# Optimization experiments

Measured on AMD Instinct MI355X. Metric: run time of the kernel, lower is better.

## Reference

```python
import jax, jax.numpy as jnp
import numpy as np

B, NO, T, SD = 2, 96, 50, 4
NE = NO * (NO - 1)            # 9120 directed edges
F, L = 64, 64                 # filter_dim, latent_dim
K, STRIDE = 8, 3              # num_time_instances, stride (hard-coded in __init__)
NW = (T - K) // STRIDE + 1    # 15 temporal windows


def swish(x):
    return x * jax.nn.sigmoid(x)


def conv1d(x, w, b):
    # x [N, Cin, T], w [Cout, Cin, k], 'same' padding as in nn.Conv1d(padding=k//2)
    k = w.shape[-1]
    y = jax.lax.conv_general_dilated(x, w, (1,), [(k // 2, k // 2)],
                                     dimension_numbers=('NCH', 'OIH', 'NCH'))
    return y + b[None, :, None]


def cond_res_block(x, latent, c1w, c1b, c2w, c2b, l1w, l1b, l2w, l2b):
    # CondResBlock1d (downsample=False): x [B*NE, F, T], latent [B, NE, L]
    l1 = latent @ l1w.T + l1b             # [B, NE, 2F]
    l2 = latent @ l2w.T + l2b
    g1, b1 = l1[..., :F], l1[..., F:]
    g2, b2 = l2[..., :F], l2[..., F:]
    t = x.shape[-1]
    h = conv1d(x, c1w, c1b).reshape(B, NE, F, t)
    h = swish(g1[..., None] * h + b1[..., None]).reshape(B * NE, F, t)
    h = conv1d(h, c2w, c2b).reshape(B, NE, F, t)
    h = swish(g2[..., None] * h + b2[..., None]).reshape(B * NE, F, t)
    return x + h


def cond_mlp_block(x, latent, f1w, f1b, f2w, f2b, l1w, l1b, l2w, l2b):
    # CondMLPResBlock1d, 3-D branch: x [B, NE, F]
    l1 = latent @ l1w.T + l1b
    l2 = latent @ l2w.T + l2b
    h = swish(l1[..., :F] * (x @ f1w.T + f1b) + l1[..., F:])
    h = swish(l2[..., :F] * (h @ f2w.T + f2b) + l2[..., F:])
    return x + h


def setup_inputs() -> dict:
    ks = iter(jax.random.split(jax.random.key(0), 40))

    def rn(shape, scale=1.0):
        return jax.random.normal(next(ks), shape, dtype=jnp.float32) * scale

    return {
        'states': rn((B, NO, T, SD)),
        'latent': rn((B, NE, L), 0.1),
        'cnnbf_w': rn((F, 2 * SD, 3), (2 * SD * 3) ** -0.5),
        'cnnbf_b': jnp.zeros((F,), jnp.float32),
        'rb_conv1_w': rn((2, F, F, 5), (F * 5) ** -0.5),
        'rb_conv1_b': jnp.zeros((2, F), jnp.float32),
        'rb_conv2_w': rn((2, F, F, 5), 1e-5),   # torch init: conv2 std=1e-5
        'rb_conv2_b': jnp.zeros((2, F), jnp.float32),
        'rb_lfc1_w': rn((2, 2 * F, L), L ** -0.5),
        'rb_lfc1_b': jnp.zeros((2, 2 * F), jnp.float32),
        'rb_lfc2_w': rn((2, 2 * F, L), L ** -0.5),
        'rb_lfc2_b': jnp.zeros((2, 2 * F), jnp.float32),
        'mlp1_fc1_w': rn((F, F * K), (F * K) ** -0.5),
        'mlp1_fc1_b': jnp.full((F,), 0.1, jnp.float32),  # MLPBlock bias fill 0.1
        'mlp1_fc2_w': rn((F, F), F ** -0.5),
        'mlp1_fc2_b': jnp.full((F,), 0.1, jnp.float32),
        'ml_fc1_w': rn((3, F, F), 1e-5),        # CondMLPResBlock fc std=1e-5
        'ml_fc1_b': jnp.zeros((3, F), jnp.float32),
        'ml_fc2_w': rn((3, F, F), 1e-5),
        'ml_fc2_b': jnp.zeros((3, F), jnp.float32),
        'ml_lfc1_w': rn((3, 2 * F, L), L ** -0.5),
        'ml_lfc1_b': jnp.zeros((3, 2 * F), jnp.float32),
        'ml_lfc2_w': rn((3, 2 * F, L), L ** -0.5),
        'ml_lfc2_b': jnp.zeros((3, 2 * F), jnp.float32),
        'em_w': rn((1, F), F ** -0.5),
        'em_b': jnp.zeros((1,), jnp.float32),
        'recv_idx': jax.random.randint(next(ks), (NE,), 0, NO, dtype=jnp.int32),
        'send_idx': jax.random.randint(next(ks), (NE,), 0, NO, dtype=jnp.int32),
    }


def reference(states, latent, cnnbf_w, cnnbf_b, rb_conv1_w, rb_conv1_b,
              rb_conv2_w, rb_conv2_b, rb_lfc1_w, rb_lfc1_b, rb_lfc2_w, rb_lfc2_b,
              mlp1_fc1_w, mlp1_fc1_b, mlp1_fc2_w, mlp1_fc2_b,
              ml_fc1_w, ml_fc1_b, ml_fc2_w, ml_fc2_b,
              ml_lfc1_w, ml_lfc1_b, ml_lfc2_w, ml_lfc2_b,
              em_w, em_b, recv_idx, send_idx):
    # node2edge gather: concat receiver/sender node trajectories -> [B, NE, T, 2*SD]
    edges = jnp.concatenate([states[:, recv_idx], states[:, send_idx]], axis=-1)
    x = edges.transpose(0, 1, 3, 2).reshape(B * NE, 2 * SD, T)
    x = swish(conv1d(x, cnnbf_w, cnnbf_b))            # [B*NE, F, T]
    for i in range(2):                                 # layer1/2_cnn_bf
        x = cond_res_block(x, latent, rb_conv1_w[i], rb_conv1_b[i],
                           rb_conv2_w[i], rb_conv2_b[i],
                           rb_lfc1_w[i], rb_lfc1_b[i], rb_lfc2_w[i], rb_lfc2_b[i])
    # temporal unfold into NW windows of K steps with stride STRIDE
    win = jnp.arange(NW)[:, None] * STRIDE + jnp.arange(K)[None, :]  # [NW, K]
    xw = x[:, :, win]                                  # [B*NE, F, NW, K]
    xw = xw.transpose(0, 2, 1, 3).reshape(B, NE, NW, F * K)
    h = swish(xw @ mlp1_fc1_w.T + mlp1_fc1_b)          # MLPBlock (eval: no dropout)
    h = (h @ mlp1_fc2_w.T + mlp1_fc2_b).mean(axis=2)   # pool windows -> [B, NE, F]
    for i in range(3):                                 # layer1/2/3
        h = cond_mlp_block(h, latent, ml_fc1_w[i], ml_fc1_b[i],
                           ml_fc2_w[i], ml_fc2_b[i],
                           ml_lfc1_w[i], ml_lfc1_b[i], ml_lfc2_w[i], ml_lfc2_b[i])
    return (h @ em_w.T + em_b)[..., 0]                 # per-edge energy [B, NE]
```

## Files before the change

kernel.cpp:

```cpp
#include <hip/hip_runtime.h>

#define B_      2
#define NO_     96
#define T_      50
#define SD_     4
#define NE_     (NO_*(NO_-1))
#define F_      64
#define NW_     15

typedef __attribute__((ext_vector_type(8))) short  short8;
typedef __attribute__((ext_vector_type(4))) float  f32x4;
typedef __attribute__((ext_vector_type(2))) float  f32x2;
typedef __attribute__((ext_vector_type(4))) unsigned short u16x4;
typedef __attribute__((ext_vector_type(2))) unsigned int   u32x2;
typedef __attribute__((ext_vector_type(4))) unsigned int   u32x4;

#define E_CONVA 0
#define E_FC1A  81920
#define E_RBL   114688
#define E_CONDP 147456
#define E_FCP   196608
#define E_C0A   225280
#define N_BF16  227328
#define HBAR_F32 115712

#define FI_FC1   10240
#define FI_RBL   14336
#define FI_CONDP 18432
#define FI_FCP   24576
#define FI_C0A   28160

#define XSTRIDE  3456
#define X0OFF    256

#define MFMA(a, b, c) __builtin_amdgcn_mfma_f32_16x16x32_bf16(a, b, c, 0, 0, 0)

__device__ __forceinline__ float swish_(float v) {
    return v * __builtin_amdgcn_rcpf(1.f + __expf(-v));
}
__device__ __forceinline__ f32x2 swish2v(f32x2 v) {
    f32x2 e;
    e.x = __expf(-v.x); e.y = __expf(-v.y);
    f32x2 d = e + (f32x2){1.f, 1.f};
    f32x2 r;
    r.x = __builtin_amdgcn_rcpf(d.x); r.y = __builtin_amdgcn_rcpf(d.y);
    return v * r;
}

__device__ __forceinline__ unsigned short f2bf(float f) {
    unsigned u = __float_as_uint(f);
    u += 0x7FFFu + ((u >> 16) & 1u);
    return (unsigned short)(u >> 16);
}
__device__ __forceinline__ float bf2f(unsigned short u) {
    return __uint_as_float(((unsigned)u) << 16);
}
__device__ __forceinline__ unsigned cvtpk(float lo, float hi) {
    unsigned r;
    asm("v_cvt_pk_bf16_f32 %0, %1, %2" : "=v"(r) : "v"(lo), "v"(hi));
    return r;
}

__global__ void prep_kernel(const float* __restrict__ cnnbf_w,
                            const float* __restrict__ rb1w, const float* __restrict__ rb2w,
                            const float* __restrict__ fc1w, const float* __restrict__ fc2w,
                            const float* __restrict__ rbl1w, const float* __restrict__ rbl2w,
                            const float* __restrict__ mll1w, const float* __restrict__ mll2w,
                            const float* __restrict__ mlf1w, const float* __restrict__ mlf2w,
                            float* __restrict__ ws) {
    int e = blockIdx.x * blockDim.x + threadIdx.x;
    if (e >= N_BF16) return;
    unsigned short* bfp = (unsigned short*)((char*)ws + 8192);
    float v;
    if (e < E_FC1A) {
        int r = e & 511, fid = e >> 9;
        int lane = r >> 3, j = r & 7;
        int kk = fid % 10, m = (fid / 10) & 3, c = fid / 40;
        int fo = m*16 + (lane & 15);
        int kidx = kk*32 + (lane >> 4)*8 + j;
        int k = kidx >> 6, fi = kidx & 63;
        int i = c >> 1;
        const float* src = (c & 1) ? rb2w : rb1w;
        v = src[((i*64 + fo)*64 + fi)*5 + k];
    } else if (e < E_RBL) {
        int e2 = e - E_FC1A;
        int r = e2 & 511, fid = e2 >> 9;
        int lane = r >> 3, j = r & 7;
        int kk = fid & 15, m = fid >> 4;
        int fo = m*16 + (lane & 15);
        int k = kk*32 + (lane >> 4)*8 + j;
        int krow = (k & 63)*8 + (k >> 6);
        v = fc1w[fo*512 + krow];
    } else if (e < E_CONDP) {
        int e3 = e - E_RBL;
        int j = e3 & 7, lane = (e3 >> 3) & 63, fid = e3 >> 9;
        int kk = fid & 1, nt = fid >> 1;
        int rb = nt >> 4, which = (nt >> 3) & 1, ot = nt & 7;
        int o = ot*16 + (lane & 15);
        int k = kk*32 + (lane >> 4)*8 + j;
        const float* src = which ? rbl2w : rbl1w;
        v = src[(rb*128 + o)*64 + k];
    } else if (e < E_FCP) {
        int e4 = e - E_CONDP;
        int r = e4 & 511, fid = e4 >> 9;
        int lane = r >> 3, j = r & 7;
        int kk = fid & 1, nt = (fid >> 1) & 15, mb = fid >> 5;
        int n = nt*16 + (lane & 15);
        int which = n >> 7, o = n & 127;
        int k = kk*32 + (lane >> 4)*8 + j;
        const float* src = which ? mll2w : mll1w;
        v = src[(mb*128 + o)*64 + k];
    } else if (e < E_C0A) {
        int e5 = e - E_FCP;
        int r = e5 & 511, fid = e5 >> 9;
        int lane = r >> 3, j = r & 7;
        int kk = fid & 1, nt = (fid >> 1) & 3, g = fid >> 3;
        int o = nt*16 + (lane & 15);
        int k = kk*32 + (lane >> 4)*8 + j;
        if (g == 0) v = fc2w[o*64 + k];
        else {
            int mb = (g - 1) >> 1;
            const float* src = ((g - 1) & 1) ? mlf2w : mlf1w;
            v = src[(mb*64 + o)*64 + k];
        }
    } else {
        int e6 = e - E_C0A;
        int j = e6 & 7, lane = (e6 >> 3) & 63, m = e6 >> 9;
        int fo = m*16 + (lane & 15);
        int k = (lane >> 4)*8 + j;
        int tap = k >> 3, fi = k & 7;
        v = (tap < 3) ? cnnbf_w[(fo*8 + fi)*3 + tap] : 0.f;
    }
    bfp[e] = f2bf(v);
}

template<bool ISCONV2>
__device__ __forceinline__ void convpass2e(const short8* __restrict__ AF, int fb,
        const unsigned short* __restrict__ Bb, unsigned short* __restrict__ Db,
        const float* __restrict__ cb,
        const float* __restrict__ gv0, const float* __restrict__ bv0,
        const float* __restrict__ gv1, const float* __restrict__ bv1,
        const int (&dixs)[2][2], const int (&ia)[10], const int (&ib)[10],
        bool skip1, int lane, int mi) {
    f32x4 acc[2][4];
#pragma unroll
    for (int ed = 0; ed < 2; ++ed)
#pragma unroll
        for (int q = 0; q < 4; ++q) acc[ed][q] = (f32x4){0.f,0.f,0.f,0.f};
#pragma unroll
    for (int kk = 0; kk < 10; ++kk) {
        short8 a0 = AF[fb + ((mi*2 + 0)*10 + kk)*64 + lane];
        short8 a1 = AF[fb + ((mi*2 + 1)*10 + kk)*64 + lane];
#pragma unroll
        for (int ed = 0; ed < 2; ++ed) {
            const unsigned short* Bs = Bb + ed*XSTRIDE;
            short8 b0 = *(const short8*)&Bs[ia[kk]];
            short8 b1 = *(const short8*)&Bs[ib[kk]];
            acc[ed][0] = MFMA(a0, b0, acc[ed][0]);
            acc[ed][1] = MFMA(a0, b1, acc[ed][1]);
            acc[ed][2] = MFMA(a1, b0, acc[ed][2]);
            acc[ed][3] = MFMA(a1, b1, acc[ed][3]);
        }
    }
#pragma unroll
    for (int ed = 0; ed < 2; ++ed) {
        const float* gv = ed ? gv1 : gv0;
        const float* bv = ed ? bv1 : bv0;
        unsigned short* Dst = Db + ed*XSTRIDE;
#pragma unroll
        for (int a = 0; a < 2; ++a) {
            const int fo0 = (mi*2 + a)*16 + ((lane >> 4))*4;
            const f32x4 cb4 = *(const f32x4*)&cb[fo0];
            const f32x4 g4  = *(const f32x4*)&gv[fo0];
            const f32x4 b4  = *(const f32x4*)&bv[fo0];
            const f32x2 glo = {g4[0], g4[1]}, ghi = {g4[2], g4[3]};
            const f32x2 gcl = __builtin_elementwise_fma(
                (f32x2){cb4[0], cb4[1]}, glo, (f32x2){b4[0], b4[1]});
            const f32x2 gch = __builtin_elementwise_fma(
                (f32x2){cb4[2], cb4[3]}, ghi, (f32x2){b4[2], b4[3]});
#pragma unroll
            for (int n = 0; n < 2; ++n) {
                if (n == 1 && skip1) continue;
                const f32x4 A = acc[ed][a*2 + n];
                f32x2 vlo = __builtin_elementwise_fma((f32x2){A[0], A[1]}, glo, gcl);
                f32x2 vhi = __builtin_elementwise_fma((f32x2){A[2], A[3]}, ghi, gch);
                f32x2 slo = swish2v(vlo);
                f32x2 shi = swish2v(vhi);
                if (ISCONV2) {
                    u16x4 old = *(u16x4*)&Dst[dixs[a][n]];
                    f32x2 olo = {bf2f(old[0]), bf2f(old[1])};
                    f32x2 ohi = {bf2f(old[2]), bf2f(old[3])};
                    slo = slo + olo; shi = shi + ohi;
                }
                *(u32x2*)&Dst[dixs[a][n]] = (u32x2){cvtpk(slo.x, slo.y),
                                                    cvtpk(shi.x, shi.y)};
            }
        }
    }
}

__global__ __launch_bounds__(256, 4) void mega_kernel(
    const float* __restrict__ states, const float* __restrict__ latent,
    const float* __restrict__ cnnbf_b,
    const float* __restrict__ rb_conv1_b, const float* __restrict__ rb_conv2_b,
    const float* __restrict__ rb_lfc1_b, const float* __restrict__ rb_lfc2_b,
    const float* __restrict__ mlp1_fc1_b,
    const int* __restrict__ recv_idx, const int* __restrict__ send_idx,
    const float* __restrict__ ws, float* __restrict__ hbar) {

    const int ge0 = blockIdx.x * 2;
    const int tid  = threadIdx.x;
    const int lane = tid & 63;
    const int wv   = tid >> 6;
    const int row0 = lane & 15, g0 = lane >> 4;
    const int mi = wv & 1, ni = wv >> 1;

    __shared__ __align__(16) unsigned short xTb[2*54*64];
    __shared__ __align__(16) unsigned short hTb[2*54*64];
    __shared__ __align__(16) unsigned short lat_bfb[2*64];
    __shared__ __align__(16) float cond_sb[2*512];

    const unsigned short* bfp = (const unsigned short*)((const char*)ws + 8192);
    const short8* AF = (const short8*)bfp;

    int dixs[2][2];
    const bool skip1 = (ni == 1) && (row0 < 14);
#pragma unroll
    for (int a = 0; a < 2; ++a) {
        const int fo0 = (mi*2 + a)*16 + g0*4;
#pragma unroll
        for (int n = 0; n < 2; ++n) {
            const int t = ((n == 0) ? ni*32 : (ni == 0 ? 16 : 34)) + row0;
            const int rw = t + 2;
            dixs[a][n] = rw*64 + ((((fo0 >> 3) ^ (rw & 7))) << 3) + (fo0 & 7);
        }
    }
    int ia[10], ib[10];
#pragma unroll
    for (int kk = 0; kk < 10; ++kk) {
        const int c  = ((kk & 1) << 2) + g0;
        const int sa = ni*32 + row0 + (kk >> 1);
        ia[kk] = sa*64 + ((c ^ (sa & 7)) << 3);
        if (ni == 0) ib[kk] = ia[kk] + 1024;
        else { const int sb2 = sa + 2; ib[kk] = sb2*64 + ((c ^ (sb2 & 7)) << 3); }
    }

    for (int z = tid; z < 512; z += 256) {
        const int edz = z >> 8, rr = (z >> 6) & 3, cc = z & 63;
        const int row = (rr < 2) ? rr : 50 + rr;
        xTb[edz*XSTRIDE + row*64 + cc] = 0;
        hTb[edz*XSTRIDE + row*64 + cc] = 0;
    }
    if (tid < 8) {
        const int edz = tid >> 2, q = tid & 3;
        const int rz = (q == 0) ? 0 : 50 + q;
        short8 zz = {0,0,0,0,0,0,0,0};
        *(short8*)&hTb[edz*XSTRIDE + X0OFF + rz*8] = zz;
    }
    const int b0_ = ge0 / NE_,       e0_ = ge0 % NE_;
    const int b1_ = (ge0+1) / NE_,   e1_ = (ge0+1) % NE_;
    const int rv0 = recv_idx[e0_], sd0 = send_idx[e0_];
    const int rv1 = recv_idx[e1_], sd1 = send_idx[e1_];
    {
        const int ed = tid >> 7, t = tid & 127;
        if (t < T_) {
            const int bsel = ed ? b1_ : b0_;
            const int rv = ed ? rv1 : rv0, sd = ed ? sd1 : sd0;
            const f32x4 r4 = *(const f32x4*)&states[((bsel*NO_ + rv)*T_ + t)*SD_];
            const f32x4 s4 = *(const f32x4*)&states[((bsel*NO_ + sd)*T_ + t)*SD_];
            u32x4 q4;
            q4[0] = cvtpk(r4[0], r4[1]); q4[1] = cvtpk(r4[2], r4[3]);
            q4[2] = cvtpk(s4[0], s4[1]); q4[3] = cvtpk(s4[2], s4[3]);
            *(u32x4*)&hTb[ed*XSTRIDE + X0OFF + (t + 1)*8] = q4;
        }
    }
    if (tid < 128) {
        const int edz = tid >> 6, c = tid & 63;
        const int bsel = edz ? b1_ : b0_, esel = edz ? e1_ : e0_;
        lat_bfb[edz*64 + c] = f2bf(latent[(bsel*NE_ + esel)*64 + c]);
    }
    __syncthreads();

    {
        const int t0a = ni * 32;
        const int sa = t0a + row0 + g0;
        const int sb = (ni == 0) ? (sa + 16) : (sa + 2);
        short8 a0 = AF[FI_C0A + (mi*2 + 0)*64 + lane];
        short8 a1 = AF[FI_C0A + (mi*2 + 1)*64 + lane];
        const f32x4 z4 = {0.f,0.f,0.f,0.f};
#pragma unroll
        for (int ed = 0; ed < 2; ++ed) {
            const unsigned short* xp = hTb + ed*XSTRIDE + X0OFF;
            short8 b0 = *(const short8*)&xp[sa * 8];
            short8 b1 = *(const short8*)&xp[sb * 8];
            f32x4 c00 = MFMA(a0, b0, z4), c01 = MFMA(a0, b1, z4);
            f32x4 c10 = MFMA(a1, b0, z4), c11 = MFMA(a1, b1, z4);
            unsigned short* xw = xTb + ed*XSTRIDE;
#pragma unroll
            for (int a = 0; a < 2; ++a) {
                const int fo0 = (mi*2 + a)*16 + g0*4;
                const f32x4 cb4 = *(const f32x4*)&cnnbf_b[fo0];
#pragma unroll
                for (int n = 0; n < 2; ++n) {
                    if (n == 1 && skip1) continue;
                    const f32x4 A = (a == 0) ? ((n == 0) ? c00 : c01)
                                             : ((n == 0) ? c10 : c11);
                    f32x2 vlo = (f32x2){A[0], A[1]} + (f32x2){cb4[0], cb4[1]};
                    f32x2 vhi = (f32x2){A[2], A[3]} + (f32x2){cb4[2], cb4[3]};
                    f32x2 slo = swish2v(vlo);
                    f32x2 shi = swish2v(vhi);
                    *(u32x2*)&xw[dixs[a][n]] = (u32x2){cvtpk(slo.x, slo.y),
                                                       cvtpk(shi.x, shi.y)};
                }
            }
        }
        short8 la0_0 = *(const short8*)&lat_bfb[g0 * 8];
        short8 la1_0 = *(const short8*)&lat_bfb[32 + g0 * 8];
        short8 la0_1 = *(const short8*)&lat_bfb[64 + g0 * 8];
        short8 la1_1 = *(const short8*)&lat_bfb[96 + g0 * 8];
        const int rbq = wv >> 1, whq = wv & 1;
        const float* cbias = (whq ? rb_lfc2_b : rb_lfc1_b) + rbq*128;
#pragma unroll
        for (int q8 = 0; q8 < 8; ++q8) {
            short8 w0 = AF[FI_RBL + ((wv*8 + q8)*2 + 0)*64 + lane];
            short8 w1 = AF[FI_RBL + ((wv*8 + q8)*2 + 1)*64 + lane];
            f32x4 d0 = MFMA(la1_0, w1, MFMA(la0_0, w0, z4));
            f32x4 d1 = MFMA(la1_1, w1, MFMA(la0_1, w0, z4));
            if (g0 == 0) {
                const int o = q8*16 + row0;
                cond_sb[rbq*256 + whq*128 + o]       = d0[0] + cbias[o];
                cond_sb[512 + rbq*256 + whq*128 + o] = d1[0] + cbias[o];
            }
        }
    }
    __syncthreads();

#pragma unroll 1
    for (int rb = 0; rb < 2; ++rb) {
        const float* c0 = cond_sb + rb*256;
        const float* c1 = cond_sb + 512 + rb*256;
        convpass2e<false>(AF, (rb*2 + 0)*2560, xTb, hTb, rb_conv1_b + rb*64,
                          c0, c0 + 64, c1, c1 + 64, dixs, ia, ib, skip1,
                          lane, mi);
        __syncthreads();
        convpass2e<true>(AF, (rb*2 + 1)*2560, hTb, xTb, rb_conv2_b + rb*64,
                         c0 + 128, c0 + 192, c1 + 128, c1 + 192, dixs, ia, ib, skip1,
                         lane, mi);
        __syncthreads();
    }

    {
        const int h = g0, nw = row0;
        f32x4 acc3[2];
        acc3[0] = (f32x4){0.f,0.f,0.f,0.f}; acc3[1] = acc3[0];
        const int nwe = (nw < 15) ? nw : 14;
        const int nwrow = 3*nwe + 2;
#pragma unroll
        for (int kk = 0; kk < 16; ++kk) {
            short8 a = AF[FI_FC1 + (wv*16 + kk)*64 + lane];
            const int row = nwrow + (kk >> 1);
            const int g   = ((kk & 1) << 2) + h;
            const int off = row*64 + ((g ^ (row & 7)) << 3);
#pragma unroll
            for (int ed = 0; ed < 2; ++ed) {
                short8 bfr = *(const short8*)&xTb[ed*XSTRIDE + off];
                acc3[ed] = MFMA(a, bfr, acc3[ed]);
            }
        }
        const f32x4 fb = *(const f32x4*)&mlp1_fc1_b[wv*16 + h*4];
#pragma unroll
        for (int ed = 0; ed < 2; ++ed) {
            f32x2 vlo = (f32x2){acc3[ed][0], acc3[ed][1]} + (f32x2){fb[0], fb[1]};
            f32x2 vhi = (f32x2){acc3[ed][2], acc3[ed][3]} + (f32x2){fb[2], fb[3]};
            f32x2 slo = swish2v(vlo);
            f32x2 shi = swish2v(vhi);
            const float sv[4] = {slo.x, slo.y, shi.x, shi.y};
            float red[4];
#pragma unroll
            for (int r = 0; r < 4; ++r) {
                float v = (nw < 15) ? sv[r] : 0.f;
                v += __shfl_xor(v, 1); v += __shfl_xor(v, 2);
                v += __shfl_xor(v, 4); v += __shfl_xor(v, 8);
                red[r] = v * (1.f / 15.f);
            }
            if (nw == 0) {
                f32x4 o4; o4[0] = red[0]; o4[1] = red[1]; o4[2] = red[2]; o4[3] = red[3];
                *(f32x4*)&hbar[(ge0 + ed)*64 + wv*16 + h*4] = o4;
            }
        }
    }
}

__global__ __launch_bounds__(256) void tail_kernel(
    const float* __restrict__ latent,
    const float* __restrict__ fc2b_g,
    const float* __restrict__ mlf1b, const float* __restrict__ mlf2b,
    const float* __restrict__ mll1b, const float* __restrict__ mll2b,
    const float* __restrict__ em_w, const float* __restrict__ em_b,
    const float* __restrict__ ws, const float* __restrict__ hbar,
    float* __restrict__ out) {

    const int m0 = blockIdx.x * 64;
    const int tid = threadIdx.x, lane = tid & 63, wv = tid >> 6;
    const int row15 = lane & 15, hgp = lane >> 4;
    const int o_l = wv*16 + row15;

    __shared__ __align__(16) unsigned short Hb[2][64*64];
    __shared__ float V[64][68];
    __shared__ float em_s[64];

    const unsigned short* bfp = (const unsigned short*)((const char*)ws + 8192);
    const short8* AFp = (const short8*)bfp;

    if (tid < 64) em_s[tid] = em_w[tid];

    {
        const int e = tid >> 2, q = tid & 3;
        const f32x4* src = (const f32x4*)&hbar[(m0 + e)*64 + q*16];
#pragma unroll
        for (int v4 = 0; v4 < 4; ++v4) {
            f32x4 x = src[v4];
            const int o0 = q*16 + v4*4;
            const int slot = o0 >> 3, half = (o0 >> 2) & 1;
            u16x4 p; p[0]=f2bf(x[0]); p[1]=f2bf(x[1]); p[2]=f2bf(x[2]); p[3]=f2bf(x[3]);
            *(u16x4*)&Hb[0][e*64 + ((slot ^ (e & 7)) << 3) + half*4] = p;
        }
    }
    __syncthreads();

    short8 lf[4][2];
#pragma unroll
    for (int m = 0; m < 4; ++m)
#pragma unroll
        for (int kk = 0; kk < 2; ++kk) {
            const float* lp = &latent[(m0 + m*16 + row15)*64 + kk*32 + hgp*8];
            f32x4 a = *(const f32x4*)lp, c = *(const f32x4*)(lp + 4);
            short8 f;
            f[0]=f2bf(a[0]); f[1]=f2bf(a[1]); f[2]=f2bf(a[2]); f[3]=f2bf(a[3]);
            f[4]=f2bf(c[0]); f[5]=f2bf(c[1]); f[6]=f2bf(c[2]); f[7]=f2bf(c[3]);
            lf[m][kk] = f;
        }

#define RD_A(buf, m, kk) \
    (*(const short8*)&Hb[buf][(m*16 + row15)*64 + ((((kk)*4 + hgp) ^ ((m*16 + row15) & 7)) << 3)])
#define RD_FCP(g, kk)  AFp[FI_FCP + (((g)*4 + wv)*2 + (kk))*64 + lane]
#define RD_CND(mb, nt, kk) AFp[FI_CONDP + (((mb)*16 + (nt))*2 + (kk))*64 + lane]

    f32x4 D[4];
#pragma unroll
    for (int m = 0; m < 4; ++m) D[m] = (f32x4){0.f,0.f,0.f,0.f};
#pragma unroll
    for (int kk = 0; kk < 2; ++kk) {
        short8 bfr = RD_FCP(0, kk);
#pragma unroll
        for (int m = 0; m < 4; ++m) D[m] = MFMA(RD_A(0, m, kk), bfr, D[m]);
    }
    {
        const float bias = fc2b_g[o_l];
#pragma unroll
        for (int m = 0; m < 4; ++m)
#pragma unroll
            for (int r = 0; r < 4; ++r) {
                const int ee = m*16 + hgp*4 + r;
                const float v = D[m][r] + bias;
                V[ee][o_l] = v;
                Hb[1][ee*64 + ((((o_l >> 3) ^ (ee & 7))) << 3) + (o_l & 7)] = f2bf(v);
            }
    }
    __syncthreads();

#pragma unroll 1
    for (int mb = 0; mb < 3; ++mb) {
        f32x4 G1[4], B1[4];
#pragma unroll
        for (int m = 0; m < 4; ++m) { G1[m] = (f32x4){0.f,0.f,0.f,0.f}; B1[m] = G1[m]; }
#pragma unroll
        for (int kk = 0; kk < 2; ++kk) {
            short8 bg = RD_CND(mb, wv,     kk);
            short8 bb = RD_CND(mb, wv + 4, kk);
#pragma unroll
            for (int m = 0; m < 4; ++m) {
                G1[m] = MFMA(lf[m][kk], bg, G1[m]);
                B1[m] = MFMA(lf[m][kk], bb, B1[m]);
            }
        }
        f32x4 D1[4];
#pragma unroll
        for (int m = 0; m < 4; ++m) D1[m] = (f32x4){0.f,0.f,0.f,0.f};
#pragma unroll
        for (int kk = 0; kk < 2; ++kk) {
            short8 bfr = RD_FCP(1 + mb*2, kk);
#pragma unroll
            for (int m = 0; m < 4; ++m) D1[m] = MFMA(RD_A(1, m, kk), bfr, D1[m]);
        }
        {
            const float bfc  = mlf1b[mb*64 + o_l];
            const float bg1  = mll1b[mb*128 + o_l];
            const float bb1  = mll1b[mb*128 + 64 + o_l];
#pragma unroll
            for (int m = 0; m < 4; ++m)
#pragma unroll
                for (int r = 0; r < 4; ++r) {
                    const int ee = m*16 + hgp*4 + r;
                    const float h1 = swish_((G1[m][r] + bg1) * (D1[m][r] + bfc)
                                            + (B1[m][r] + bb1));
                    Hb[0][ee*64 + ((((o_l >> 3) ^ (ee & 7))) << 3) + (o_l & 7)] = f2bf(h1);
                }
        }
        __syncthreads();

        f32x4 G2[4], B2[4];
#pragma unroll
        for (int m = 0; m < 4; ++m) { G2[m] = (f32x4){0.f,0.f,0.f,0.f}; B2[m] = G2[m]; }
#pragma unroll
        for (int kk = 0; kk < 2; ++kk) {
            short8 bg = RD_CND(mb, wv + 8,  kk);
            short8 bb = RD_CND(mb, wv + 12, kk);
#pragma unroll
            for (int m = 0; m < 4; ++m) {
                G2[m] = MFMA(lf[m][kk], bg, G2[m]);
                B2[m] = MFMA(lf[m][kk], bb, B2[m]);
            }
        }
        f32x4 D2[4];
#pragma unroll
        for (int m = 0; m < 4; ++m) D2[m] = (f32x4){0.f,0.f,0.f,0.f};
#pragma unroll
        for (int kk = 0; kk < 2; ++kk) {
            short8 bfr = RD_FCP(2 + mb*2, kk);
#pragma unroll
            for (int m = 0; m < 4; ++m) D2[m] = MFMA(RD_A(0, m, kk), bfr, D2[m]);
        }
        {
            const float bfc  = mlf2b[mb*64 + o_l];
            const float bg2  = mll2b[mb*128 + o_l];
            const float bb2  = mll2b[mb*128 + 64 + o_l];
#pragma unroll
            for (int m = 0; m < 4; ++m)
#pragma unroll
                for (int r = 0; r < 4; ++r) {
                    const int ee = m*16 + hgp*4 + r;
                    const float add = swish_((G2[m][r] + bg2) * (D2[m][r] + bfc)
                                             + (B2[m][r] + bb2));
                    const float vn = V[ee][o_l] + add;
                    V[ee][o_l] = vn;
                    Hb[1][ee*64 + ((((o_l >> 3) ^ (ee & 7))) << 3) + (o_l & 7)] = f2bf(vn);
                }
        }
        __syncthreads();
    }

    if (tid < 64) {
        const int ee = tid;
        float acc = em_b[0];
#pragma unroll 16
        for (int j = 0; j < 64; ++j) {
            const int o = (j + ee) & 63;
            acc += V[ee][o] * em_s[o];
        }
        out[m0 + ee] = acc;
    }
}

extern "C" void kernel_launch(void* const* d_in, const int* in_sizes, int n_in,
                              void* d_out, int out_size, void* d_ws, size_t ws_size,
                              hipStream_t stream) {
    const float* states   = (const float*)d_in[0];
    const float* latent   = (const float*)d_in[1];
    const float* cnnbf_w  = (const float*)d_in[2];
    const float* cnnbf_b  = (const float*)d_in[3];
    const float* rb1w     = (const float*)d_in[4];
    const float* rb1b     = (const float*)d_in[5];
    const float* rb2w     = (const float*)d_in[6];
    const float* rb2b     = (const float*)d_in[7];
    const float* rbl1w    = (const float*)d_in[8];
    const float* rbl1b    = (const float*)d_in[9];
    const float* rbl2w    = (const float*)d_in[10];
    const float* rbl2b    = (const float*)d_in[11];
    const float* fc1w     = (const float*)d_in[12];
    const float* fc1b     = (const float*)d_in[13];
    const float* fc2w     = (const float*)d_in[14];
    const float* fc2b     = (const float*)d_in[15];
    const float* mlf1w    = (const float*)d_in[16];
    const float* mlf1b    = (const float*)d_in[17];
    const float* mlf2w    = (const float*)d_in[18];
    const float* mlf2b    = (const float*)d_in[19];
    const float* mll1w    = (const float*)d_in[20];
    const float* mll1b    = (const float*)d_in[21];
    const float* mll2w    = (const float*)d_in[22];
    const float* mll2b    = (const float*)d_in[23];
    const float* em_w     = (const float*)d_in[24];
    const float* em_b     = (const float*)d_in[25];
    const int*   recv_idx = (const int*)d_in[26];
    const int*   send_idx = (const int*)d_in[27];
    float* ws  = (float*)d_ws;
    float* out = (float*)d_out;
    float* hbar = ws + HBAR_F32;

    prep_kernel<<<(N_BF16 + 255) / 256, 256, 0, stream>>>(
        cnnbf_w, rb1w, rb2w, fc1w, fc2w, rbl1w, rbl2w, mll1w, mll2w, mlf1w, mlf2w, ws);

    mega_kernel<<<B_ * NE_ / 2, 256, 0, stream>>>(
        states, latent, cnnbf_b, rb1b, rb2b, rbl1b, rbl2b, fc1b,
        recv_idx, send_idx, ws, hbar);

    tail_kernel<<<(B_ * NE_) / 64, 256, 0, stream>>>(
        latent, fc2b, mlf1b, mlf2b, mll1b, mll2b, em_w, em_b, ws, hbar, out);
}
```

Baseline: 295.2 us.

## Assign each wave one edge and all output channels in conv passes

Reassigns the block's four waves so each computes all 64 output channels for a single edge and time half, instead of half the channels for both edges. Each kk step now loads four weight fragments from global memory and two activation fragments from LDS, instead of two and four. The aim is to cut LDS reads of the activation tiles and simplify indexing. The cost is doubled weight-fragment traffic from cache and more per-lane index registers.

```diff
diff --git a/kernel.cpp b/kernel.cpp
--- a/kernel.cpp
+++ b/kernel.cpp
@@ -135,66 +135,56 @@
 }
 
 template<bool ISCONV2>
-__device__ __forceinline__ void convpass2e(const short8* __restrict__ AF, int fb,
-        const unsigned short* __restrict__ Bb, unsigned short* __restrict__ Db,
+__device__ __forceinline__ void convpass4m(const short8* __restrict__ AF, int fb,
+        const unsigned short* __restrict__ Bs, unsigned short* __restrict__ Dst,
         const float* __restrict__ cb,
-        const float* __restrict__ gv0, const float* __restrict__ bv0,
-        const float* __restrict__ gv1, const float* __restrict__ bv1,
-        const int (&dixs)[2][2], const int (&ia)[10], const int (&ib)[10],
-        bool skip1, int lane, int mi) {
-    f32x4 acc[2][4];
-#pragma unroll
-    for (int ed = 0; ed < 2; ++ed)
-#pragma unroll
-        for (int q = 0; q < 4; ++q) acc[ed][q] = (f32x4){0.f,0.f,0.f,0.f};
+        const float* __restrict__ gv, const float* __restrict__ bv,
+        const int (&dixs)[4][2], const int (&ia)[10], const int (&ib)[10],
+        bool skip1, int lane, int g0) {
+    f32x4 acc[4][2];
+#pragma unroll
+    for (int m = 0; m < 4; ++m) {
+        acc[m][0] = (f32x4){0.f,0.f,0.f,0.f};
+        acc[m][1] = acc[m][0];
+    }
 #pragma unroll
     for (int kk = 0; kk < 10; ++kk) {
-        short8 a0 = AF[fb + ((mi*2 + 0)*10 + kk)*64 + lane];
-        short8 a1 = AF[fb + ((mi*2 + 1)*10 + kk)*64 + lane];
-#pragma unroll
-        for (int ed = 0; ed < 2; ++ed) {
-            const unsigned short* Bs = Bb + ed*XSTRIDE;
-            short8 b0 = *(const short8*)&Bs[ia[kk]];
-            short8 b1 = *(const short8*)&Bs[ib[kk]];
-            acc[ed][0] = MFMA(a0, b0, acc[ed][0]);
-            acc[ed][1] = MFMA(a0, b1, acc[ed][1]);
-            acc[ed][2] = MFMA(a1, b0, acc[ed][2]);
-            acc[ed][3] = MFMA(a1, b1, acc[ed][3]);
-        }
-    }
-#pragma unroll
-    for (int ed = 0; ed < 2; ++ed) {
-        const float* gv = ed ? gv1 : gv0;
-        const float* bv = ed ? bv1 : bv0;
-        unsigned short* Dst = Db + ed*XSTRIDE;
-#pragma unroll
-        for (int a = 0; a < 2; ++a) {
-            const int fo0 = (mi*2 + a)*16 + ((lane >> 4))*4;
-            const f32x4 cb4 = *(const f32x4*)&cb[fo0];
-            const f32x4 g4  = *(const f32x4*)&gv[fo0];
-            const f32x4 b4  = *(const f32x4*)&bv[fo0];
-            const f32x2 glo = {g4[0], g4[1]}, ghi = {g4[2], g4[3]};
-            const f32x2 gcl = __builtin_elementwise_fma(
-                (f32x2){cb4[0], cb4[1]}, glo, (f32x2){b4[0], b4[1]});
-            const f32x2 gch = __builtin_elementwise_fma(
-                (f32x2){cb4[2], cb4[3]}, ghi, (f32x2){b4[2], b4[3]});
-#pragma unroll
-            for (int n = 0; n < 2; ++n) {
-                if (n == 1 && skip1) continue;
-                const f32x4 A = acc[ed][a*2 + n];
-                f32x2 vlo = __builtin_elementwise_fma((f32x2){A[0], A[1]}, glo, gcl);
-                f32x2 vhi = __builtin_elementwise_fma((f32x2){A[2], A[3]}, ghi, gch);
-                f32x2 slo = swish2v(vlo);
-                f32x2 shi = swish2v(vhi);
-                if (ISCONV2) {
-                    u16x4 old = *(u16x4*)&Dst[dixs[a][n]];
-                    f32x2 olo = {bf2f(old[0]), bf2f(old[1])};
-                    f32x2 ohi = {bf2f(old[2]), bf2f(old[3])};
-                    slo = slo + olo; shi = shi + ohi;
-                }
-                *(u32x2*)&Dst[dixs[a][n]] = (u32x2){cvtpk(slo.x, slo.y),
-                                                    cvtpk(shi.x, shi.y)};
-            }
+        short8 b0 = *(const short8*)&Bs[ia[kk]];
+        short8 b1 = *(const short8*)&Bs[ib[kk]];
+#pragma unroll
+        for (int m = 0; m < 4; ++m) {
+            short8 am = AF[fb + (m*10 + kk)*64 + lane];
+            acc[m][0] = MFMA(am, b0, acc[m][0]);
+            acc[m][1] = MFMA(am, b1, acc[m][1]);
+        }
+    }
+#pragma unroll
+    for (int m = 0; m < 4; ++m) {
+        const int fo0 = m*16 + g0*4;
+        const f32x4 cb4 = *(const f32x4*)&cb[fo0];
+        const f32x4 g4  = *(const f32x4*)&gv[fo0];
+        const f32x4 b4  = *(const f32x4*)&bv[fo0];
+        const f32x2 glo = {g4[0], g4[1]}, ghi = {g4[2], g4[3]};
+        const f32x2 gcl = __builtin_elementwise_fma(
+            (f32x2){cb4[0], cb4[1]}, glo, (f32x2){b4[0], b4[1]});
+        const f32x2 gch = __builtin_elementwise_fma(
+            (f32x2){cb4[2], cb4[3]}, ghi, (f32x2){b4[2], b4[3]});
+#pragma unroll
+        for (int n = 0; n < 2; ++n) {
+            if (n == 1 && skip1) continue;
+            const f32x4 A = acc[m][n];
+            f32x2 vlo = __builtin_elementwise_fma((f32x2){A[0], A[1]}, glo, gcl);
+            f32x2 vhi = __builtin_elementwise_fma((f32x2){A[2], A[3]}, ghi, gch);
+            f32x2 slo = swish2v(vlo);
+            f32x2 shi = swish2v(vhi);
+            if (ISCONV2) {
+                u16x4 old = *(u16x4*)&Dst[dixs[m][n]];
+                f32x2 olo = {bf2f(old[0]), bf2f(old[1])};
+                f32x2 ohi = {bf2f(old[2]), bf2f(old[3])};
+                slo = slo + olo; shi = shi + ohi;
+            }
+            *(u32x2*)&Dst[dixs[m][n]] = (u32x2){cvtpk(slo.x, slo.y),
+                                                cvtpk(shi.x, shi.y)};
         }
     }
 }
@@ -213,7 +203,7 @@
     const int lane = tid & 63;
     const int wv   = tid >> 6;
     const int row0 = lane & 15, g0 = lane >> 4;
-    const int mi = wv & 1, ni = wv >> 1;
+    const int ed = wv & 1, ni = wv >> 1;
 
     __shared__ __align__(16) unsigned short xTb[2*54*64];
     __shared__ __align__(16) unsigned short hTb[2*54*64];
@@ -223,16 +213,16 @@
     const unsigned short* bfp = (const unsigned short*)((const char*)ws + 8192);
     const short8* AF = (const short8*)bfp;
 
-    int dixs[2][2];
+    int dixs[4][2];
     const bool skip1 = (ni == 1) && (row0 < 14);
 #pragma unroll
-    for (int a = 0; a < 2; ++a) {
-        const int fo0 = (mi*2 + a)*16 + g0*4;
+    for (int m = 0; m < 4; ++m) {
+        const int fo0 = m*16 + g0*4;
 #pragma unroll
         for (int n = 0; n < 2; ++n) {
             const int t = ((n == 0) ? ni*32 : (ni == 0 ? 16 : 34)) + row0;
             const int rw = t + 2;
-            dixs[a][n] = rw*64 + ((((fo0 >> 3) ^ (rw & 7))) << 3) + (fo0 & 7);
+            dixs[m][n] = rw*64 + ((((fo0 >> 3) ^ (rw & 7))) << 3) + (fo0 & 7);
         }
     }
     int ia[10], ib[10];
@@ -262,16 +252,16 @@
     const int rv0 = recv_idx[e0_], sd0 = send_idx[e0_];
     const int rv1 = recv_idx[e1_], sd1 = send_idx[e1_];
     {
-        const int ed = tid >> 7, t = tid & 127;
+        const int edg = tid >> 7, t = tid & 127;
         if (t < T_) {
-            const int bsel = ed ? b1_ : b0_;
-            const int rv = ed ? rv1 : rv0, sd = ed ? sd1 : sd0;
+            const int bsel = edg ? b1_ : b0_;
+            const int rv = edg ? rv1 : rv0, sd = edg ? sd1 : sd0;
             const f32x4 r4 = *(const f32x4*)&states[((bsel*NO_ + rv)*T_ + t)*SD_];
             const f32x4 s4 = *(const f32x4*)&states[((bsel*NO_ + sd)*T_ + t)*SD_];
             u32x4 q4;
             q4[0] = cvtpk(r4[0], r4[1]); q4[1] = cvtpk(r4[2], r4[3]);
             q4[2] = cvtpk(s4[0], s4[1]); q4[3] = cvtpk(s4[2], s4[3]);
-            *(u32x4*)&hTb[ed*XSTRIDE + X0OFF + (t + 1)*8] = q4;
+            *(u32x4*)&hTb[edg*XSTRIDE + X0OFF + (t + 1)*8] = q4;
         }
     }
     if (tid < 128) {
@@ -282,36 +272,30 @@
     __syncthreads();
 
     {
-        const int t0a = ni * 32;
-        const int sa = t0a + row0 + g0;
+        const int sa = ni*32 + row0 + g0;
         const int sb = (ni == 0) ? (sa + 16) : (sa + 2);
-        short8 a0 = AF[FI_C0A + (mi*2 + 0)*64 + lane];
-        short8 a1 = AF[FI_C0A + (mi*2 + 1)*64 + lane];
         const f32x4 z4 = {0.f,0.f,0.f,0.f};
-#pragma unroll
-        for (int ed = 0; ed < 2; ++ed) {
-            const unsigned short* xp = hTb + ed*XSTRIDE + X0OFF;
-            short8 b0 = *(const short8*)&xp[sa * 8];
-            short8 b1 = *(const short8*)&xp[sb * 8];
-            f32x4 c00 = MFMA(a0, b0, z4), c01 = MFMA(a0, b1, z4);
-            f32x4 c10 = MFMA(a1, b0, z4), c11 = MFMA(a1, b1, z4);
-            unsigned short* xw = xTb + ed*XSTRIDE;
-#pragma unroll
-            for (int a = 0; a < 2; ++a) {
-                const int fo0 = (mi*2 + a)*16 + g0*4;
-                const f32x4 cb4 = *(const f32x4*)&cnnbf_b[fo0];
-#pragma unroll
-                for (int n = 0; n < 2; ++n) {
-                    if (n == 1 && skip1) continue;
-                    const f32x4 A = (a == 0) ? ((n == 0) ? c00 : c01)
-                                             : ((n == 0) ? c10 : c11);
-                    f32x2 vlo = (f32x2){A[0], A[1]} + (f32x2){cb4[0], cb4[1]};
-                    f32x2 vhi = (f32x2){A[2], A[3]} + (f32x2){cb4[2], cb4[3]};
-                    f32x2 slo = swish2v(vlo);
-                    f32x2 shi = swish2v(vhi);
-                    *(u32x2*)&xw[dixs[a][n]] = (u32x2){cvtpk(slo.x, slo.y),
-                                                       cvtpk(shi.x, shi.y)};
-                }
+        const unsigned short* xp = hTb + ed*XSTRIDE + X0OFF;
+        short8 b0 = *(const short8*)&xp[sa * 8];
+        short8 b1 = *(const short8*)&xp[sb * 8];
+        unsigned short* xw = xTb + ed*XSTRIDE;
+#pragma unroll
+        for (int m = 0; m < 4; ++m) {
+            short8 am = AF[FI_C0A + m*64 + lane];
+            f32x4 cA = MFMA(am, b0, z4);
+            f32x4 cB = MFMA(am, b1, z4);
+            const int fo0 = m*16 + g0*4;
+            const f32x4 cb4 = *(const f32x4*)&cnnbf_b[fo0];
+#pragma unroll
+            for (int n = 0; n < 2; ++n) {
+                if (n == 1 && skip1) continue;
+                const f32x4 A = (n == 0) ? cA : cB;
+                f32x2 vlo = (f32x2){A[0], A[1]} + (f32x2){cb4[0], cb4[1]};
+                f32x2 vhi = (f32x2){A[2], A[3]} + (f32x2){cb4[2], cb4[3]};
+                f32x2 slo = swish2v(vlo);
+                f32x2 shi = swish2v(vhi);
+                *(u32x2*)&xw[dixs[m][n]] = (u32x2){cvtpk(slo.x, slo.y),
+                                                   cvtpk(shi.x, shi.y)};
             }
         }
         short8 la0_0 = *(const short8*)&lat_bfb[g0 * 8];
@@ -324,8 +308,10 @@
         for (int q8 = 0; q8 < 8; ++q8) {
             short8 w0 = AF[FI_RBL + ((wv*8 + q8)*2 + 0)*64 + lane];
             short8 w1 = AF[FI_RBL + ((wv*8 + q8)*2 + 1)*64 + lane];
-            f32x4 d0 = MFMA(la1_0, w1, MFMA(la0_0, w0, z4));
-            f32x4 d1 = MFMA(la1_1, w1, MFMA(la0_1, w0, z4));
+            f32x4 t0 = MFMA(la0_0, w0, z4);
+            f32x4 d0 = MFMA(la1_0, w1, t0);
+            f32x4 t1 = MFMA(la0_1, w0, z4);
+            f32x4 d1 = MFMA(la1_1, w1, t1);
             if (g0 == 0) {
                 const int o = q8*16 + row0;
                 cond_sb[rbq*256 + whq*128 + o]       = d0[0] + cbias[o];
@@ -337,15 +323,14 @@
 
 #pragma unroll 1
     for (int rb = 0; rb < 2; ++rb) {
-        const float* c0 = cond_sb + rb*256;
-        const float* c1 = cond_sb + 512 + rb*256;
-        convpass2e<false>(AF, (rb*2 + 0)*2560, xTb, hTb, rb_conv1_b + rb*64,
-                          c0, c0 + 64, c1, c1 + 64, dixs, ia, ib, skip1,
-                          lane, mi);
+        const float* ce = cond_sb + ed*512 + rb*256;
+        convpass4m<false>(AF, (rb*2 + 0)*2560, xTb + ed*XSTRIDE, hTb + ed*XSTRIDE,
+                          rb_conv1_b + rb*64, ce, ce + 64, dixs, ia, ib, skip1,
+                          lane, g0);
         __syncthreads();
-        convpass2e<true>(AF, (rb*2 + 1)*2560, hTb, xTb, rb_conv2_b + rb*64,
-                         c0 + 128, c0 + 192, c1 + 128, c1 + 192, dixs, ia, ib, skip1,
-                         lane, mi);
+        convpass4m<true>(AF, (rb*2 + 1)*2560, hTb + ed*XSTRIDE, xTb + ed*XSTRIDE,
+                         rb_conv2_b + rb*64, ce + 128, ce + 192, dixs, ia, ib, skip1,
+                         lane, g0);
         __syncthreads();
     }
 
@@ -362,16 +347,16 @@
             const int g   = ((kk & 1) << 2) + h;
             const int off = row*64 + ((g ^ (row & 7)) << 3);
 #pragma unroll
-            for (int ed = 0; ed < 2; ++ed) {
-                short8 bfr = *(const short8*)&xTb[ed*XSTRIDE + off];
-                acc3[ed] = MFMA(a, bfr, acc3[ed]);
+            for (int edx = 0; edx < 2; ++edx) {
+                short8 bfr = *(const short8*)&xTb[edx*XSTRIDE + off];
+                acc3[edx] = MFMA(a, bfr, acc3[edx]);
             }
         }
         const f32x4 fb = *(const f32x4*)&mlp1_fc1_b[wv*16 + h*4];
 #pragma unroll
-        for (int ed = 0; ed < 2; ++ed) {
-            f32x2 vlo = (f32x2){acc3[ed][0], acc3[ed][1]} + (f32x2){fb[0], fb[1]};
-            f32x2 vhi = (f32x2){acc3[ed][2], acc3[ed][3]} + (f32x2){fb[2], fb[3]};
+        for (int edx = 0; edx < 2; ++edx) {
+            f32x2 vlo = (f32x2){acc3[edx][0], acc3[edx][1]} + (f32x2){fb[0], fb[1]};
+            f32x2 vhi = (f32x2){acc3[edx][2], acc3[edx][3]} + (f32x2){fb[2], fb[3]};
             f32x2 slo = swish2v(vlo);
             f32x2 shi = swish2v(vhi);
             const float sv[4] = {slo.x, slo.y, shi.x, shi.y};
@@ -385,7 +370,7 @@
             }
             if (nw == 0) {
                 f32x4 o4; o4[0] = red[0]; o4[1] = red[1]; o4[2] = red[2]; o4[3] = red[3];
-                *(f32x4*)&hbar[(ge0 + ed)*64 + wv*16 + h*4] = o4;
+                *(f32x4*)&hbar[(ge0 + edx)*64 + wv*16 + h*4] = o4;
             }
         }
     }
```

Result: slower. 366.9 us (+24.3%).
